# Kernel tuning notes

Measured on AMD Instinct MI355X. Metric: run time of the kernel, lower is better.

Reference implementation:

```python
import jax, jax.numpy as jnp
import numpy as np

# iRPE contextual+transposed, method=PRODUCT, rpe config ratio=1.9
ALPHA, BETA, GAMMA = 1.9, 3.8, 15.2
BETA_INT = int(BETA)            # 3
S = 2 * BETA_INT + 1            # 7
NUM_BUCKETS = S * S             # 49
B, H, D = 8, 8, 64
HEIGHT = WIDTH = 32
L = HEIGHT * WIDTH              # 1024, skip = L - height*width = 0


def _piecewise_index(rp):
    # numpy port of torch piecewise_index (no-grad, precomputed constant)
    rp = np.asarray(rp)
    rp_abs = np.abs(rp)
    safe = np.maximum(rp_abs.astype(np.float64), ALPHA)  # avoid log(0) under mask
    y = ALPHA + np.log(safe / ALPHA) / np.log(GAMMA / ALPHA) * (BETA - ALPHA)
    y = np.minimum(np.round(y), BETA)                    # round then clip(max=beta)
    out = np.where(rp_abs <= ALPHA, np.round(rp.astype(np.float64)), np.sign(rp) * y)
    return out.astype(np.int64)                          # trunc toward zero (+-3.8 -> +-3)


def _rp_bucket_product(height, width):
    pos = np.stack(np.meshgrid(np.arange(height), np.arange(width), indexing='ij'), -1)
    pos = pos.reshape(-1, 2)                             # (L, 2)
    diff = pos[:, None, :] - pos[None, :, :]             # (L, L, 2)
    r = _piecewise_index(diff[:, :, 0]) + BETA_INT
    c = _piecewise_index(diff[:, :, 1]) + BETA_INT
    return (r * S + c).astype(np.int32)                  # values in [0, 49)


def setup_inputs() -> dict:
    key = jax.random.key(0)
    k1, k2 = jax.random.split(key)
    x = jax.random.normal(k1, (B, H, L, D), dtype=jnp.float32)
    lookup_table_weight = jax.random.normal(k2, (H, D, NUM_BUCKETS), dtype=jnp.float32) * 0.02
    rp_bucket = jnp.asarray(_rp_bucket_product(HEIGHT, WIDTH))  # (L, L) int32 constant
    return {"x": x, "lookup_table_weight": lookup_table_weight, "rp_bucket": rp_bucket}


def reference(x, lookup_table_weight, rp_bucket):
    # x: (B, H, L, D); lookup_table_weight: (H, D, K); rp_bucket: (L, L) int
    # lt[b,h,l,k] = sum_d x[b,h,l,d] * W[h,d,k]
    lt = jnp.einsum('bhld,hdk->bhlk', x, lookup_table_weight)  # (B, H, L, K) small
    Lq = rp_bucket.shape[0]
    row = jnp.arange(Lq)[:, None]                              # (L, 1)
    # out[b,h,i,j] = lt[b,h,i,rp_bucket[i,j]] -- the big irregular gather
    return lt[:, :, row, rp_bucket]                            # (B, H, L, L)
```

## Files before the change

### kernel.cpp

```cpp
#include <hip/hip_runtime.h>


constexpr int cB = 8;
constexpr int cH = 8;
constexpr int cL = 1024;
constexpr int cD = 64;
constexpr int cK = 49;

__global__ __launch_bounds__(256) void irpe_kernel(
    const float* __restrict__ x,
    const float* __restrict__ W,
    const int*   __restrict__ bucket,
    float*       __restrict__ out)
{
    __shared__ float xs[cD];
    __shared__ float lt_row[cK];

    const int gid = blockIdx.x;
    const int i   = gid >> 6;
    const int bh  = gid & 63;
    const int h   = bh & 7;

    const int tid = threadIdx.x;

    if (tid < cD) {
        xs[tid] = x[((size_t)bh * cL + i) * cD + tid];
    }
    __syncthreads();

    if (tid < cK) {
        const float* wp = W + (size_t)h * cD * cK + tid;
        float acc = 0.0f;
        #pragma unroll
        for (int d = 0; d < cD; ++d) {
            acc = fmaf(xs[d], wp[(size_t)d * cK], acc);
        }
        lt_row[tid] = acc;
    }
    __syncthreads();

    const int4* brow = (const int4*)(bucket + (size_t)i * cL);
    float4*     orow = (float4*)(out + ((size_t)bh * cL + i) * cL);

    const int4 bk = brow[tid];
    float4 o;
    o.x = lt_row[bk.x];
    o.y = lt_row[bk.y];
    o.z = lt_row[bk.z];
    o.w = lt_row[bk.w];
    orow[tid] = o;
}

extern "C" void kernel_launch(void* const* d_in, const int* in_sizes, int n_in,
                              void* d_out, int out_size, void* d_ws, size_t ws_size,
                              hipStream_t stream) {
    const float* x      = (const float*)d_in[0];
    const float* W      = (const float*)d_in[1];
    const int*   bucket = (const int*)d_in[2];
    float*       out    = (float*)d_out;

    const int grid = cB * cH * cL;
    irpe_kernel<<<grid, 256, 0, stream>>>(x, W, bucket, out);
}
```

Before: 349.1 us.

## Process 32 batch-heads per block to reuse bucket row and amortize setup

Measured after the change: 320.4 us. -8.2%, faster.

```diff
diff --git a/kernel.cpp b/kernel.cpp
--- a/kernel.cpp
+++ b/kernel.cpp
@@ -1,54 +1,66 @@
 #include <hip/hip_runtime.h>
 
 
-constexpr int cB = 8;
-constexpr int cH = 8;
 constexpr int cL = 1024;
 constexpr int cD = 64;
 constexpr int cK = 49;
+constexpr int cBH = 64;
+constexpr int cHALF = 32;
 
-__global__ __launch_bounds__(256) void irpe_kernel(
+__global__ __launch_bounds__(256) void irpe_fused(
     const float* __restrict__ x,
     const float* __restrict__ W,
     const int*   __restrict__ bucket,
     float*       __restrict__ out)
 {
-    __shared__ float xs[cD];
-    __shared__ float lt_row[cK];
+    __shared__ float4 xs4[cHALF][cD / 4];
+    __shared__ float  lts[cHALF * cK];
 
-    const int gid = blockIdx.x;
-    const int i   = gid >> 6;
-    const int bh  = gid & 63;
-    const int h   = bh & 7;
+    const int gid  = blockIdx.x;
+    const int i    = gid >> 1;
+    const int bh0  = (gid & 1) * cHALF;
+    const int tid  = threadIdx.x;
 
-    const int tid = threadIdx.x;
+    const float4* x4 = (const float4*)x;
+    #pragma unroll
+    for (int r = 0; r < 2; ++r) {
+        const int idx = r * 256 + tid;
+        const int lh  = idx >> 4;
+        const int d4  = idx & 15;
+        xs4[lh][d4] = x4[((size_t)(bh0 + lh) * cL + i) * (cD / 4) + d4];
+    }
 
-    if (tid < cD) {
-        xs[tid] = x[((size_t)bh * cL + i) * cD + tid];
+    const int4 bk = ((const int4*)(bucket + (size_t)i * cL))[tid];
+
+    __syncthreads();
+
+    const float* xsf = (const float*)xs4;
+    for (int p = tid; p < cHALF * cK; p += 256) {
+        const int lh = p / cK;
+        const int k  = p - lh * cK;
+        const int h  = (bh0 + lh) & 7;
+        const float* wp = W + (size_t)h * cD * cK + k;
+        const float* xr = xsf + lh * cD;
+        float acc = 0.0f;
+        #pragma unroll
+        for (int d = 0; d < cD; ++d) {
+            acc = fmaf(xr[d], wp[(size_t)d * cK], acc);
+        }
+        lts[p] = acc;
     }
     __syncthreads();
 
-    if (tid < cK) {
-        const float* wp = W + (size_t)h * cD * cK + tid;
-        float acc = 0.0f;
-        #pragma unroll
-        for (int d = 0; d < cD; ++d) {
-            acc = fmaf(xs[d], wp[(size_t)d * cK], acc);
-        }
-        lt_row[tid] = acc;
+    float4* obase = (float4*)(out + (size_t)bh0 * cL * cL + (size_t)i * cL);
+    #pragma unroll 4
+    for (int lh = 0; lh < cHALF; ++lh) {
+        const float* lrow = lts + lh * cK;
+        float4 o;
+        o.x = lrow[bk.x];
+        o.y = lrow[bk.y];
+        o.z = lrow[bk.z];
+        o.w = lrow[bk.w];
+        obase[(size_t)lh * cL * (cL / 4) + tid] = o;
     }
-    __syncthreads();
-
-    const int4* brow = (const int4*)(bucket + (size_t)i * cL);
-    float4*     orow = (float4*)(out + ((size_t)bh * cL + i) * cL);
-
-    const int4 bk = brow[tid];
-    float4 o;
-    o.x = lt_row[bk.x];
-    o.y = lt_row[bk.y];
-    o.z = lt_row[bk.z];
-    o.w = lt_row[bk.w];
-    orow[tid] = o;
 }
 
 extern "C" void kernel_launch(void* const* d_in, const int* in_sizes, int n_in,
@@ -59,6 +71,6 @@
     const int*   bucket = (const int*)d_in[2];
     float*       out    = (float*)d_out;
 
-    const int grid = cB * cH * cL;
-    irpe_kernel<<<grid, 256, 0, stream>>>(x, W, bucket, out);
+    const int grid = cL * 2;
+    irpe_fused<<<grid, 256, 0, stream>>>(x, W, bucket, out);
 }
```

## Process all batch-heads per query row with register-held weights in one block

Applied to the files above, without the earlier changes.

Measured after the change: 331.9 us. 1.05x faster.

```diff
diff --git a/kernel.cpp b/kernel.cpp
--- a/kernel.cpp
+++ b/kernel.cpp
@@ -1,54 +1,59 @@
 #include <hip/hip_runtime.h>
 
 
-constexpr int cB = 8;
-constexpr int cH = 8;
 constexpr int cL = 1024;
 constexpr int cD = 64;
 constexpr int cK = 49;
 
-__global__ __launch_bounds__(256) void irpe_kernel(
+typedef float vf4 __attribute__((ext_vector_type(4)));
+
+__global__ __launch_bounds__(512, 4) void irpe_fused(
     const float* __restrict__ x,
     const float* __restrict__ W,
     const int*   __restrict__ bucket,
     float*       __restrict__ out)
 {
-    __shared__ float xs[cD];
-    __shared__ float lt_row[cK];
+    __shared__ float sc[8][64];
 
-    const int gid = blockIdx.x;
-    const int i   = gid >> 6;
-    const int bh  = gid & 63;
-    const int h   = bh & 7;
+    const int gid  = blockIdx.x;
+    const int i    = ((gid & 255) << 2) | (gid >> 8);
+    const int tid  = threadIdx.x;
+    const int lane = tid & 63;
+    const int w    = tid >> 6;
 
-    const int tid = threadIdx.x;
+    const int kc = lane < cK ? lane : (cK - 1);
+    const float* wb = W + (size_t)w * cD * cK + kc;
+    float wr[cD];
+    #pragma unroll
+    for (int d = 0; d < cD; ++d)
+        wr[d] = wb[(size_t)d * cK];
 
-    if (tid < cD) {
-        xs[tid] = x[((size_t)bh * cL + i) * cD + tid];
-    }
-    __syncthreads();
+    const int4* brow = (const int4*)(bucket + (size_t)i * cL);
 
-    if (tid < cK) {
-        const float* wp = W + (size_t)h * cD * cK + tid;
+    for (int q = 0; q < 8; ++q) {
+        const int bh = q * 8 + w;
+
+        const float* xr = x + ((size_t)bh * cL + i) * cD;
         float acc = 0.0f;
         #pragma unroll
-        for (int d = 0; d < cD; ++d) {
-            acc = fmaf(xs[d], wp[(size_t)d * cK], acc);
+        for (int d = 0; d < cD; ++d)
+            acc = fmaf(xr[d], wr[d], acc);
+
+        sc[w][lane] = acc;
+
+        vf4* orow = (vf4*)(out + ((size_t)bh * cL + i) * cL);
+        #pragma unroll
+        for (int t = 0; t < 4; ++t) {
+            const int4 bk = brow[t * 64 + lane];
+            const float* s = sc[w];
+            vf4 o;
+            o.x = s[bk.x];
+            o.y = s[bk.y];
+            o.z = s[bk.z];
+            o.w = s[bk.w];
+            __builtin_nontemporal_store(o, &orow[t * 64 + lane]);
         }
-        lt_row[tid] = acc;
     }
-    __syncthreads();
-
-    const int4* brow = (const int4*)(bucket + (size_t)i * cL);
-    float4*     orow = (float4*)(out + ((size_t)bh * cL + i) * cL);
-
-    const int4 bk = brow[tid];
-    float4 o;
-    o.x = lt_row[bk.x];
-    o.y = lt_row[bk.y];
-    o.z = lt_row[bk.z];
-    o.w = lt_row[bk.w];
-    orow[tid] = o;
 }
 
 extern "C" void kernel_launch(void* const* d_in, const int* in_sizes, int n_in,
@@ -59,6 +64,5 @@
     const int*   bucket = (const int*)d_in[2];
     float*       out    = (float*)d_out;
 
-    const int grid = cB * cH * cL;
-    irpe_kernel<<<grid, 256, 0, stream>>>(x, W, bucket, out);
+    irpe_fused<<<cL, 512, 0, stream>>>(x, W, bucket, out);
 }
```
